# Kernel tuning notes

Hardware: AMD Instinct MI355X
Metric: run time of the kernel (lower is better)

The kernel has to match this reference:

```python
import jax, jax.numpy as jnp
import numpy as np
import math

H = 128
HEADS = 2
NEG = -float(1 << 32)
BN_EPS = 1e-5
LN_EPS = 1e-5


def _bn_eval(x, g, b):
    # BatchNorm1d in eval mode with running_mean=0, running_var=1
    return g * (x / jnp.sqrt(1.0 + BN_EPS)) + b


def _ln(x, g, b):
    mu = x.mean(-1, keepdims=True)
    var = ((x - mu) ** 2).mean(-1, keepdims=True)
    return g * (x - mu) / jnp.sqrt(var + LN_EPS) + b


def _multi_embed(tables, idx):
    # tables [F,V,H], idx [N,F] -> sum_f tables[f, idx[:,f]]  (ogb Atom/BondEncoder)
    F = tables.shape[0]
    return tables[jnp.arange(F)[None, :], idx].sum(axis=1)


def _gin_graph(x, edge_attr, edge_index, batch, num_graphs, atom_emb, bond_emb, eps, w1, b1, g1, be1, w2, b2, g2, be2):
    h = _multi_embed(atom_emb, x)  # [N,H]
    tgt, src = edge_index[0], edge_index[1]
    L = eps.shape[0]
    for l in range(L):
        e = _multi_embed(bond_emb[l], edge_attr)  # [E,H]
        msg = jax.nn.relu(h[src] + e)
        agg = jax.ops.segment_sum(msg, tgt, num_segments=h.shape[0])
        z = (1.0 + eps[l]) * h + agg
        z = jax.nn.relu(_bn_eval(z @ w1[l] + b1[l], g1[l], be1[l])) @ w2[l] + b2[l]
        h = _bn_eval(z, g2[l], be2[l])
        if l != L - 1:
            h = jax.nn.relu(h)  # dropout is identity in eval mode
    s = jax.ops.segment_sum(h, batch, num_segments=num_graphs)
    c = jax.ops.segment_sum(jnp.ones_like(h), batch, num_segments=num_graphs)
    return s / (c + 1e-9)  # mean pooling per graph


def _sab(X, wq, bq, wk, bk, wv, bv, wo, bo, l1g, l1b, l2g, l2b):
    # MAB(X, X) with HEADS heads, use_ln=True. X: [B,S,H]
    B, S, _ = X.shape
    dh = H // HEADS

    def split(T):  # torch split(last)+cat(dim0): head-major [HEADS*B, S, dh]
        return T.reshape(B, S, HEADS, dh).transpose(2, 0, 1, 3).reshape(HEADS * B, S, dh)

    Qs, Ks, Vs = split(X @ wq + bq), split(X @ wk + bk), split(X @ wv + bv)
    A = jax.nn.softmax(jnp.einsum('bqd,bkd->bqk', Qs, Ks) / math.sqrt(dh), axis=-1)
    O = Qs + jnp.einsum('bqk,bkd->bqd', A, Vs)
    O = O.reshape(HEADS, B, S, dh).transpose(1, 2, 0, 3).reshape(B, S, H)
    O = _ln(O, l1g, l1b)
    O = _ln(O @ wo + bo, l2g, l2b)
    return O


def setup_inputs() -> dict:
    key = jax.random.key(0)
    ks = iter(jax.random.split(key, 64))
    nk = lambda: next(ks)
    V, L = 64, 4
    NS, ES = 60000, 140000
    NM, EM = 150000, 350000
    S, M, D, B = 492, 600, 200, 64
    f32 = jnp.float32
    w = lambda *shp: jax.random.normal(nk(), shp, f32) * 0.05
    inp = {}
    inp['atom_emb'] = w(2, 9, V, H)
    inp['bond_emb'] = w(2, L, 3, V, H)
    inp['gin_eps'] = jnp.zeros((2, L), f32)
    inp['gin_w1'] = w(2, L, H, 2 * H); inp['gin_b1'] = jnp.zeros((2, L, 2 * H), f32)
    inp['gin_bn1_g'] = jnp.ones((2, L, 2 * H), f32); inp['gin_bn1_b'] = jnp.zeros((2, L, 2 * H), f32)
    inp['gin_w2'] = w(2, L, 2 * H, H); inp['gin_b2'] = jnp.zeros((2, L, H), f32)
    inp['gin_bn2_g'] = jnp.ones((2, L, H), f32); inp['gin_bn2_b'] = jnp.zeros((2, L, H), f32)
    for nm in ['sab_wq', 'sab_wk', 'sab_wv', 'sab_wo']:
        inp[nm] = w(H, H)
    for nm in ['sab_bq', 'sab_bk', 'sab_bv', 'sab_bo', 'sab_ln1_b', 'sab_ln2_b']:
        inp[nm] = jnp.zeros((H,), f32)
    inp['sab_ln1_g'] = jnp.ones((H,), f32); inp['sab_ln2_g'] = jnp.ones((H,), f32)
    inp['agg_wq'] = w(H, H); inp['agg_bq'] = jnp.zeros((H,), f32)
    inp['agg_wk'] = w(H, H); inp['agg_bk'] = jnp.zeros((H,), f32)
    inp['score_w1'] = w(H, H // 2); inp['score_b1'] = jnp.zeros((H // 2,), f32)
    inp['score_w2'] = w(H // 2, 1); inp['score_b2'] = jnp.zeros((1,), f32)
    inp['patient_emb'] = jax.random.uniform(nk(), (B, S), f32)
    inp['average_projection'] = jax.random.uniform(nk(), (D, M), f32) / M
    inp['sub_x'] = jax.random.randint(nk(), (NS, 9), 0, V)
    inp['sub_edge_attr'] = jax.random.randint(nk(), (ES, 3), 0, V)
    inp['sub_edge_index'] = jax.random.randint(nk(), (2, ES), 0, NS)
    inp['sub_batch'] = jax.random.randint(nk(), (NS,), 0, S)
    inp['mol_x'] = jax.random.randint(nk(), (NM, 9), 0, V)
    inp['mol_edge_attr'] = jax.random.randint(nk(), (EM, 3), 0, V)
    inp['mol_edge_index'] = jax.random.randint(nk(), (2, EM), 0, NM)
    inp['mol_batch'] = jax.random.randint(nk(), (NM,), 0, M)
    mask = jax.random.bernoulli(nk(), 0.3, (D, S))
    inp['mask'] = mask.at[:, 0].set(False)
    inp['num_sub'] = S
    inp['num_mol'] = M
    return inp


def reference(atom_emb, bond_emb, gin_eps, gin_w1, gin_b1, gin_bn1_g, gin_bn1_b, gin_w2, gin_b2, gin_bn2_g, gin_bn2_b, sab_wq, sab_bq, sab_wk, sab_bk, sab_wv, sab_bv, sab_wo, sab_bo, sab_ln1_g, sab_ln1_b, sab_ln2_g, sab_ln2_b, agg_wq, agg_bq, agg_wk, agg_bk, score_w1, score_b1, score_w2, score_b2, patient_emb, average_projection, sub_x, sub_edge_attr, sub_edge_index, sub_batch, mol_x, mol_edge_attr, mol_edge_index, mol_batch, mask, num_sub, num_mol):
    # substructure encoder (GINGraph #0) + SAB interaction
    sub = _gin_graph(sub_x, sub_edge_attr, sub_edge_index, sub_batch, num_sub, atom_emb[0], bond_emb[0], gin_eps[0], gin_w1[0], gin_b1[0], gin_bn1_g[0], gin_bn1_b[0], gin_w2[0], gin_b2[0], gin_bn2_g[0], gin_bn2_b[0])
    sub = _sab(sub[None], sab_wq, sab_bq, sab_wk, sab_bk, sab_wv, sab_bv, sab_wo, sab_bo, sab_ln1_g, sab_ln1_b, sab_ln2_g, sab_ln2_b)[0]  # [S,H]
    # molecule encoder (GINGraph #1) + drug-level averaging
    mol = _gin_graph(mol_x, mol_edge_attr, mol_edge_index, mol_batch, num_mol, atom_emb[1], bond_emb[1], gin_eps[1], gin_w1[1], gin_b1[1], gin_bn1_g[1], gin_bn1_b[1], gin_w2[1], gin_b2[1], gin_bn2_g[1], gin_bn2_b[1])
    mol_emb = average_projection @ mol  # [D,H]
    # AttnAgg: masked attention, per-patient reweighting via diag(fix_feat)
    Q = mol_emb @ agg_wq + agg_bq
    K = sub @ agg_wk + agg_bk
    attn = (Q @ K.T) / math.sqrt(H)
    attn = jax.nn.softmax(jnp.where(mask, NEG, attn), axis=-1)  # [D,S]
    agg = jnp.einsum('ds,bs,sh->bdh', attn, patient_emb, sub)  # [B,D,H]
    logits = (jax.nn.relu(agg @ score_w1 + score_b1) @ score_w2 + score_b2)[..., 0]
    return jax.nn.sigmoid(logits)  # y_prob [B,D]
```

## Files before the change

kernel.cpp:

```cpp
#include <hip/hip_runtime.h>


typedef short short8 __attribute__((ext_vector_type(8)));
typedef unsigned short us8 __attribute__((ext_vector_type(8)));
typedef float f32x4 __attribute__((ext_vector_type(4)));
typedef unsigned short us4 __attribute__((ext_vector_type(4)));
typedef unsigned int u32;

#define BN_RSQ 0.9999950000374997f
#define LN_EPS 1e-5f
#define NEGBIG -4294967296.0f

__device__ __forceinline__ unsigned short f2bf(float x) {
  union { float f; unsigned int u; } v; v.f = x;
  unsigned int r = v.u + 0x7fffu + ((v.u >> 16) & 1u);
  return (unsigned short)(r >> 16);
}
__device__ __forceinline__ float bf2f(unsigned short x) {
  union { unsigned int u; float f; } v; v.u = ((unsigned int)x) << 16;
  return v.f;
}

__global__ __launch_bounds__(256) void prep_all(
    const float* __restrict__ w1, const float* __restrict__ w2,
    unsigned short* __restrict__ w1t, unsigned short* __restrict__ w2t,
    const float* __restrict__ bond, unsigned short* __restrict__ bt16, int bonde,
    const unsigned char* __restrict__ m, int* __restrict__ flags, int maskn) {
  __shared__ int lf[2];
  int b = blockIdx.x;
  if (b < 1024) {
    int i = b * 256 + threadIdx.x;
    int gl = i >> 15;
    int k1 = (i >> 8) & 127, c1 = i & 255;
    w1t[(gl << 15) + c1 * 128 + k1] = f2bf(w1[i]);
    int k2 = (i >> 7) & 255, c2 = i & 127;
    w2t[(gl << 15) + c2 * 256 + k2] = f2bf(w2[i]);
    return;
  }
  if (b < 1792) {
    int i = (b - 1024) * 256 + threadIdx.x;
    if (i < bonde) bt16[i] = f2bf(bond[i]);
    return;
  }
  if (threadIdx.x == 0) { lf[0] = 0; lf[1] = 0; }
  __syncthreads();
  int f0 = 0, f1 = 0;
  for (int i = (b - 1792) * 256 + threadIdx.x; i < maskn; i += 64 * 256) {
    if (m[i]) { if ((i & 3) == 0) f0 = 1; else f1 = 1; }
  }
  if (f0) atomicOr(&lf[0], 1);
  if (f1) atomicOr(&lf[1], 1);
  __syncthreads();
  if (threadIdx.x == 0) {
    if (lf[0]) atomicOr(flags, 1);
    if (lf[1]) atomicOr(flags + 1, 1);
  }
}

__global__ void build_count(const int* __restrict__ ei_m, int Em,
                            const int* __restrict__ ei_s, int Es,
                            const int* __restrict__ bm, int Nm,
                            const int* __restrict__ bs, int Ns,
                            int* __restrict__ deg_e, int* __restrict__ deg_n,
                            int M, int NmR) {
  int i = blockIdx.x * 256 + threadIdx.x;
  if (i < Em) { atomicAdd(&deg_e[ei_m[i]], 1); return; }
  i -= Em;
  if (i < Es) { atomicAdd(&deg_e[NmR + ei_s[i]], 1); return; }
  i -= Es;
  if (i < Nm) { atomicAdd(&deg_n[bm[i]], 1); return; }
  i -= Nm;
  if (i < Ns) { atomicAdd(&deg_n[M + bs[i]], 1); }
}

__global__ __launch_bounds__(256) void scan_block2(
    const int* __restrict__ cntE, int nE, int* __restrict__ exclE, int* __restrict__ bsumE, int nbE,
    const int* __restrict__ cntN, int nN, int* __restrict__ exclN, int* __restrict__ bsumN) {
  const int* cnt; int n; int* excl; int* bsum; int blk;
  if (blockIdx.x < (unsigned)nbE) { cnt = cntE; n = nE; excl = exclE; bsum = bsumE; blk = blockIdx.x; }
  else { cnt = cntN; n = nN; excl = exclN; bsum = bsumN; blk = blockIdx.x - nbE; }
  int gid = blk * 256 + threadIdx.x;
  int lane = threadIdx.x & 63, w = threadIdx.x >> 6;
  int v = (gid < n) ? cnt[gid] : 0;
  int x = v;
#pragma unroll
  for (int off = 1; off < 64; off <<= 1) {
    int y = __shfl_up(x, off, 64);
    if (lane >= off) x += y;
  }
  __shared__ int wt[4];
  if (lane == 63) wt[w] = x;
  __syncthreads();
  int add = 0;
  for (int i = 0; i < w; i++) add += wt[i];
  x += add;
  if (gid < n) excl[gid] = x - v;
  if (threadIdx.x == 255) bsum[blk] = x;
}

__global__ __launch_bounds__(1024) void scan_top2(int* __restrict__ bsumE, int nE,
                                                  int* __restrict__ bsumN, int nN) {
  int* bsum = blockIdx.x ? bsumN : bsumE;
  int n = blockIdx.x ? nN : nE;
  int t = threadIdx.x;
  int lane = t & 63, w = t >> 6;
  int v = (t < n) ? bsum[t] : 0;
  int x = v;
#pragma unroll
  for (int off = 1; off < 64; off <<= 1) {
    int y = __shfl_up(x, off, 64);
    if (lane >= off) x += y;
  }
  __shared__ int wt[16];
  if (lane == 63) wt[w] = x;
  __syncthreads();
  int add = 0;
  for (int i = 0; i < w; i++) add += wt[i];
  x += add;
  if (t < n) bsum[t] = x - v;
}

__global__ void finalize2(const int* __restrict__ exclE, const int* __restrict__ bsumE,
                          int nE, int totE, int* __restrict__ rowE,
                          const int* __restrict__ exclN, const int* __restrict__ bsumN,
                          int nN, int totN, int* __restrict__ rowN) {
  int i = blockIdx.x * 256 + threadIdx.x;
  if (i <= nE) {
    rowE[i] = (i < nE) ? (exclE[i] + bsumE[i >> 8]) : totE;
    return;
  }
  int j = i - nE - 1;
  if (j <= nN) rowN[j] = (j < nN) ? (exclN[j] + bsumN[j >> 8]) : totN;
}

__global__ void scatter2(const int* __restrict__ ei_m, const int* __restrict__ ea_m, int Em,
                         const int* __restrict__ ei_s, const int* __restrict__ ea_s, int Es, int NmR,
                         const int* __restrict__ rowptr_e, int* __restrict__ cur_e,
                         int2* __restrict__ epool,
                         const int* __restrict__ bm, int Nm,
                         const int* __restrict__ bs, int Ns, int M,
                         const int* __restrict__ rowptr_n, int* __restrict__ cur_n,
                         int* __restrict__ npool) {
  int i = blockIdx.x * 256 + threadIdx.x;
  if (i < Em + Es) {
    int g, src, a0, a1, a2;
    if (i < Em) {
      g = ei_m[i]; src = ei_m[Em + i];
      a0 = ea_m[i * 3]; a1 = ea_m[i * 3 + 1]; a2 = ea_m[i * 3 + 2];
    } else {
      int j = i - Em;
      g = NmR + ei_s[j]; src = NmR + ei_s[Es + j];
      a0 = ea_s[j * 3]; a1 = ea_s[j * 3 + 1]; a2 = ea_s[j * 3 + 2];
    }
    int slot = rowptr_e[g] + atomicAdd(&cur_e[g], 1);
    epool[slot] = make_int2(src * 128, a0 | (a1 << 6) | (a2 << 12));
    return;
  }
  int k = i - (Em + Es);
  if (k >= Nm + Ns) return;
  int g, node;
  if (k < Nm) { g = bm[k]; node = k; }
  else { int j = k - Nm; g = M + bs[j]; node = NmR + j; }
  int slot = rowptr_n[g] + atomicAdd(&cur_n[g], 1);
  npool[slot] = node;
}

__global__ void embed2(const int* __restrict__ xm, const int* __restrict__ xs,
                       const float* __restrict__ atab, int Nm, int Ns, int NmR,
                       unsigned short* __restrict__ h) {
  int i = blockIdx.x * 256 + threadIdx.x;
  const int* x; const float* table; int n, cq, outn;
  if (i < Nm * 32) {
    n = i >> 5; cq = (i & 31) * 4; x = xm; table = atab + (size_t)9 * 64 * 128; outn = n;
  } else {
    int j = i - Nm * 32;
    if (j >= Ns * 32) return;
    n = j >> 5; cq = (j & 31) * 4; x = xs; table = atab; outn = NmR + n;
  }
  float4 s = make_float4(0.f, 0.f, 0.f, 0.f);
#pragma unroll
  for (int f = 0; f < 9; f++) {
    int v = x[n * 9 + f];
    float4 tv = *(const float4*)(table + (size_t)(f * 64 + v) * 128 + cq);
    s.x += tv.x; s.y += tv.y; s.z += tv.z; s.w += tv.w;
  }
  us4 o;
  o.x = f2bf(s.x); o.y = f2bf(s.y); o.z = f2bf(s.z); o.w = f2bf(s.w);
  *(us4*)(h + (size_t)outn * 128 + cq) = o;
}

__global__ __launch_bounds__(256, 4) void gin_fused3(
    const unsigned short* __restrict__ hin, unsigned short* __restrict__ hout,
    const float* __restrict__ eps_all, int l, int NmR,
    const unsigned short* __restrict__ bt16,
    const int2* __restrict__ epool, const int* __restrict__ rowptr_e,
    const unsigned short* __restrict__ w1t_a, const float* __restrict__ b1_a,
    const float* __restrict__ g1_a, const float* __restrict__ be1_a,
    const unsigned short* __restrict__ w2t_a, const float* __restrict__ b2_a,
    const float* __restrict__ g2_a, const float* __restrict__ be2_a) {
  __shared__ __align__(16) unsigned char smem[38144];
  unsigned short* z1s = (unsigned short*)smem;
  unsigned short* zs  = (unsigned short*)(smem + 20736);
  int2* recs = (int2*)smem;
  const int CAP = 2592;
  int t = threadIdx.x;
  int r0 = blockIdx.x * 64;
  int g = (r0 < NmR) ? 1 : 0;
  int gl = g * 4 + l;
  const unsigned short* bt = bt16 + (size_t)gl * 3 * 64 * 128;
  const unsigned short* w1t = w1t_a + (size_t)gl * 32768;
  const unsigned short* w2t = w2t_a + (size_t)gl * 32768;
  const float* b1 = b1_a + gl * 256;
  const float* g1 = g1_a + gl * 256;
  const float* be1 = be1_a + gl * 256;
  const float* b2 = b2_a + gl * 128;
  const float* g2 = g2_a + gl * 128;
  const float* be2 = be2_a + gl * 128;
  float eps1 = 1.0f + eps_all[gl];
  int do_relu = (l != 3);

  int e0 = rowptr_e[r0], e1 = rowptr_e[r0 + 64];
  int nE = e1 - e0;
  int nstage = (nE < CAP) ? nE : CAP;
  for (int i = t; i < nstage; i += 256) recs[i] = epool[e0 + i];
  __syncthreads();

#pragma unroll
  for (int p = 0; p < 2; p++) {
    int lr = p * 32 + (t >> 3);
    int n = r0 + lr;
    int cb = (t & 7) * 16;
    float lo[8], hi[8];
    {
      const u32* hr = (const u32*)(hin + (size_t)n * 128 + cb);
      uint4 h0v = *(const uint4*)hr;
      uint4 h1v = *(const uint4*)(hr + 4);
      u32 hd[8] = {h0v.x, h0v.y, h0v.z, h0v.w, h1v.x, h1v.y, h1v.z, h1v.w};
#pragma unroll
      for (int j = 0; j < 8; j++) {
        lo[j] = eps1 * __uint_as_float(hd[j] << 16);
        hi[j] = eps1 * __uint_as_float(hd[j] & 0xffff0000u);
      }
    }
    int le0 = rowptr_e[n] - e0, le1 = rowptr_e[n + 1] - e0;
    for (int li = le0; li < le1; li++) {
      int2 rec = (li < CAP) ? recs[li] : epool[e0 + li];
      u32 ab = (u32)rec.y;
      const u32* hs = (const u32*)(hin + rec.x + cb);
      const u32* q0 = (const u32*)(bt + (ab & 63u) * 128 + cb);
      const u32* q1 = (const u32*)(bt + (64 + ((ab >> 6) & 63u)) * 128 + cb);
      const u32* q2 = (const u32*)(bt + (128 + ((ab >> 12) & 63u)) * 128 + cb);
      uint4 A0 = *(const uint4*)hs, A1 = *(const uint4*)(hs + 4);
      uint4 B0 = *(const uint4*)q0, B1 = *(const uint4*)(q0 + 4);
      uint4 C0 = *(const uint4*)q1, C1 = *(const uint4*)(q1 + 4);
      uint4 D0 = *(const uint4*)q2, D1 = *(const uint4*)(q2 + 4);
      u32 ad[8] = {A0.x, A0.y, A0.z, A0.w, A1.x, A1.y, A1.z, A1.w};
      u32 bd[8] = {B0.x, B0.y, B0.z, B0.w, B1.x, B1.y, B1.z, B1.w};
      u32 cd[8] = {C0.x, C0.y, C0.z, C0.w, C1.x, C1.y, C1.z, C1.w};
      u32 dd[8] = {D0.x, D0.y, D0.z, D0.w, D1.x, D1.y, D1.z, D1.w};
#pragma unroll
      for (int j = 0; j < 8; j++) {
        float sl = __uint_as_float(ad[j] << 16) + __uint_as_float(bd[j] << 16)
                 + __uint_as_float(cd[j] << 16) + __uint_as_float(dd[j] << 16);
        float sh = __uint_as_float(ad[j] & 0xffff0000u) + __uint_as_float(bd[j] & 0xffff0000u)
                 + __uint_as_float(cd[j] & 0xffff0000u) + __uint_as_float(dd[j] & 0xffff0000u);
        lo[j] += fmaxf(sl, 0.f);
        hi[j] += fmaxf(sh, 0.f);
      }
    }
    u32 od[8];
#pragma unroll
    for (int j = 0; j < 8; j++)
      od[j] = (u32)f2bf(lo[j]) | (((u32)f2bf(hi[j])) << 16);
    u32* zr = (u32*)(zs + lr * 136 + cb);
    *(uint4*)zr = make_uint4(od[0], od[1], od[2], od[3]);
    *(uint4*)(zr + 4) = make_uint4(od[4], od[5], od[6], od[7]);
  }
  __syncthreads();

  int lane = t & 63, wave = t >> 6;
  int quad = lane >> 4, l16 = lane & 15;
  {
    short8 bw[4][4];
    int cb = wave * 64;
#pragma unroll
    for (int nt = 0; nt < 4; nt++) {
      const unsigned short* p = w1t + (cb + nt * 16 + l16) * 128 + quad * 8;
#pragma unroll
      for (int kc = 0; kc < 4; kc++) bw[nt][kc] = *(const short8*)(p + kc * 32);
    }
    for (int mt = 0; mt < 4; mt++) {
      short8 af[4];
      const unsigned short* zrow = zs + (mt * 16 + l16) * 136 + quad * 8;
#pragma unroll
      for (int kc = 0; kc < 4; kc++)
        af[kc] = *(const short8*)(zrow + kc * 32);
#pragma unroll
      for (int nt = 0; nt < 4; nt++) {
        f32x4 acc = {0.f, 0.f, 0.f, 0.f};
#pragma unroll
        for (int kc = 0; kc < 4; kc++)
          acc = __builtin_amdgcn_mfma_f32_16x16x32_bf16(af[kc], bw[nt][kc], acc, 0, 0, 0);
        int c = cb + nt * 16 + l16;
        float sc = g1[c] * BN_RSQ, sh = be1[c], bb = b1[c];
#pragma unroll
        for (int reg = 0; reg < 4; reg++) {
          int r = mt * 16 + quad * 4 + reg;
          float y = (acc[reg] + bb) * sc + sh;
          z1s[r * 264 + c] = f2bf(fmaxf(y, 0.f));
        }
      }
      __syncthreads();
    }
  }
  {
    short8 bw[2][8];
    int cb = wave * 32;
#pragma unroll
    for (int nt = 0; nt < 2; nt++) {
      const unsigned short* p = w2t + (cb + nt * 16 + l16) * 256 + quad * 8;
#pragma unroll
      for (int kc = 0; kc < 8; kc++) bw[nt][kc] = *(const short8*)(p + kc * 32);
    }
    for (int mt = 0; mt < 4; mt++) {
      short8 af[8];
      const unsigned short* zrow = z1s + (mt * 16 + l16) * 264 + quad * 8;
#pragma unroll
      for (int kc = 0; kc < 8; kc++)
        af[kc] = *(const short8*)(zrow + kc * 32);
      __syncthreads();
#pragma unroll
      for (int nt = 0; nt < 2; nt++) {
        f32x4 acc = {0.f, 0.f, 0.f, 0.f};
#pragma unroll
        for (int kc = 0; kc < 8; kc++)
          acc = __builtin_amdgcn_mfma_f32_16x16x32_bf16(af[kc], bw[nt][kc], acc, 0, 0, 0);
        int c = cb + nt * 16 + l16;
        float sc = g2[c] * BN_RSQ, sh = be2[c], bb = b2[c];
#pragma unroll
        for (int reg = 0; reg < 4; reg++) {
          int r = mt * 16 + quad * 4 + reg;
          float y = (acc[reg] + bb) * sc + sh;
          if (do_relu) y = fmaxf(y, 0.f);
          z1s[r * 264 + c] = f2bf(y);
        }
      }
    }
  }
  __syncthreads();
  for (int i = t; i < 1024; i += 256) {
    int r = i >> 4, c8 = (i & 15) * 8;
    us8 v = *(const us8*)(z1s + r * 264 + c8);
    *(us8*)(hout + (size_t)(r0 + r) * 128 + c8) = v;
  }
}

__global__ __launch_bounds__(256) void pool_csr(const unsigned short* __restrict__ h,
                                                const int* __restrict__ npool,
                                                const int* __restrict__ rowptr_n,
                                                float* __restrict__ pooled, int nseg) {
  __shared__ int nls[512];
  __shared__ float part[128];
  int m = blockIdx.x;
  if (m >= nseg) return;
  int st = rowptr_n[m];
  int len = rowptr_n[m + 1] - st;
  int c = threadIdx.x & 127, grp = threadIdx.x >> 7;
  float s = 0.f;
  for (int base = 0; base < len; base += 512) {
    int cnt = (len - base < 512) ? (len - base) : 512;
    __syncthreads();
    for (int i = threadIdx.x; i < cnt; i += 256) nls[i] = npool[st + base + i];
    __syncthreads();
    int hh = (cnt + 1) >> 1;
    int i0 = grp * hh;
    int i1 = i0 + hh; if (i1 > cnt) i1 = cnt;
    int i = i0;
    for (; i + 3 < i1; i += 4) {
      int n0 = nls[i], n1 = nls[i + 1], n2 = nls[i + 2], n3 = nls[i + 3];
      float v0 = bf2f(h[(size_t)n0 * 128 + c]);
      float v1 = bf2f(h[(size_t)n1 * 128 + c]);
      float v2 = bf2f(h[(size_t)n2 * 128 + c]);
      float v3 = bf2f(h[(size_t)n3 * 128 + c]);
      s += (v0 + v1) + (v2 + v3);
    }
    for (; i < i1; i++) s += bf2f(h[(size_t)nls[i] * 128 + c]);
  }
  if (grp) part[c] = s;
  __syncthreads();
  if (!grp) pooled[(size_t)m * 128 + c] = (s + part[c]) / ((float)len + 1e-9f);
}

__global__ __launch_bounds__(256) void gemm_tile(const float* __restrict__ A, const float* __restrict__ W,
                                                 const float* __restrict__ bias, float* __restrict__ C,
                                                 int K) {
  __shared__ float As[608];
  __shared__ float red[128];
  int r = blockIdx.x;
  int t = threadIdx.x;
  for (int i = t; i < K; i += 256) As[i] = A[(size_t)r * K + i];
  __syncthreads();
  int c = t & 127, half = t >> 7;
  int Kh = K >> 1;
  int k0 = half * Kh, k1 = k0 + Kh;
  float acc = 0.f;
#pragma unroll 8
  for (int k = k0; k < k1; k++) acc = fmaf(As[k], W[(size_t)k * 128 + c], acc);
  if (half) red[c] = acc;
  __syncthreads();
  if (!half) {
    float v = acc + red[c] + (bias ? bias[c] : 0.f);
    C[(size_t)r * 128 + c] = v;
  }
}

__global__ __launch_bounds__(256) void gemm_qkv(const float* __restrict__ A,
                                                const float* __restrict__ W0, const float* __restrict__ bi0, float* __restrict__ C0,
                                                const float* __restrict__ W1, const float* __restrict__ bi1, float* __restrict__ C1,
                                                const float* __restrict__ W2, const float* __restrict__ bi2, float* __restrict__ C2) {
  __shared__ float As[128];
  __shared__ float red[128];
  int r = blockIdx.x, which = blockIdx.y;
  const float* W = (which == 0) ? W0 : (which == 1) ? W1 : W2;
  const float* bias = (which == 0) ? bi0 : (which == 1) ? bi1 : bi2;
  float* C = (which == 0) ? C0 : (which == 1) ? C1 : C2;
  int t = threadIdx.x;
  if (t < 128) As[t] = A[(size_t)r * 128 + t];
  __syncthreads();
  int c = t & 127, half = t >> 7;
  int k0 = half * 64, k1 = k0 + 64;
  float acc = 0.f;
#pragma unroll 8
  for (int k = k0; k < k1; k++) acc = fmaf(As[k], W[(size_t)k * 128 + c], acc);
  if (half) red[c] = acc;
  __syncthreads();
  if (!half) C[(size_t)r * 128 + c] = acc + red[c] + bias[c];
}

__global__ __launch_bounds__(256) void gemm_aggqk(
    const float* __restrict__ Aq, const float* __restrict__ Wq, const float* __restrict__ bq,
    float* __restrict__ Cq, int D,
    const float* __restrict__ Ak, const float* __restrict__ Wk, const float* __restrict__ bk,
    float* __restrict__ Ck) {
  __shared__ float As[128];
  __shared__ float red[128];
  int r = blockIdx.x;
  const float* A; const float* W; const float* bias; float* C; int rr;
  if (r < D) { A = Aq; W = Wq; bias = bq; C = Cq; rr = r; }
  else { A = Ak; W = Wk; bias = bk; C = Ck; rr = r - D; }
  int t = threadIdx.x;
  if (t < 128) As[t] = A[(size_t)rr * 128 + t];
  __syncthreads();
  int c = t & 127, half = t >> 7;
  int k0 = half * 64, k1 = k0 + 64;
  float acc = 0.f;
#pragma unroll 8
  for (int k = k0; k < k1; k++) acc = fmaf(As[k], W[(size_t)k * 128 + c], acc);
  if (half) red[c] = acc;
  __syncthreads();
  if (!half) C[(size_t)rr * 128 + c] = acc + red[c] + bias[c];
}

__global__ __launch_bounds__(256) void gemm_wo_ln(const float* __restrict__ A,
                                                  const float* __restrict__ W, const float* __restrict__ bias,
                                                  const float* __restrict__ lg, const float* __restrict__ lb,
                                                  float* __restrict__ subf,
                                                  unsigned short* __restrict__ subT) {
  __shared__ float As[128];
  __shared__ float row[128];
  __shared__ float red2[4];
  int r = blockIdx.x;
  int t = threadIdx.x;
  if (t < 128) As[t] = A[(size_t)r * 128 + t];
  __syncthreads();
  int c = t & 127, half = t >> 7;
  int k0 = half * 64, k1 = k0 + 64;
  float acc = 0.f;
#pragma unroll 8
  for (int k = k0; k < k1; k++) acc = fmaf(As[k], W[(size_t)k * 128 + c], acc);
  if (half) row[c] = acc;
  __syncthreads();
  if (!half) row[c] = acc + row[c] + bias[c];
  __syncthreads();
  if (t < 128) {
    float x = row[t];
    float s = x;
    for (int off = 32; off; off >>= 1) s += __shfl_down(s, off);
    if ((t & 63) == 0) red2[t >> 6] = s;
  }
  __syncthreads();
  if (t < 128) {
    float mu = (red2[0] + red2[1]) * (1.f / 128.f);
    float dd = row[t] - mu;
    float v = dd * dd;
    for (int off = 32; off; off >>= 1) v += __shfl_down(v, off);
    if ((t & 63) == 0) red2[2 + (t >> 6)] = v;
  }
  __syncthreads();
  if (t < 128) {
    float mu = (red2[0] + red2[1]) * (1.f / 128.f);
    float var = (red2[2] + red2[3]) * (1.f / 128.f);
    float dd = row[t] - mu;
    float val = lg[t] * dd * rsqrtf(var + LN_EPS) + lb[t];
    subf[(size_t)r * 128 + t] = val;
    subT[(size_t)t * 512 + r] = f2bf(val);
  }
}

__global__ __launch_bounds__(256) void sab_attn(const float* __restrict__ Q, const float* __restrict__ K,
                                                const float* __restrict__ V, float* __restrict__ O, int S) {
  int q = blockIdx.x, hd = blockIdx.y;
  int t = threadIdx.x;
  __shared__ float sc[512];
  __shared__ float red[8];
  __shared__ float pacc[4][64];
  const float* qrow = Q + q * 128 + hd * 64;
  for (int k = t; k < 512; k += 256) {
    float d = -1e30f;
    if (k < S) {
      const float* krow = K + k * 128 + hd * 64;
      d = 0.f;
#pragma unroll
      for (int j = 0; j < 64; j += 4) {
        float4 a = *(const float4*)(qrow + j);
        float4 b = *(const float4*)(krow + j);
        d += a.x * b.x + a.y * b.y + a.z * b.z + a.w * b.w;
      }
      d *= 0.125f;
    }
    sc[k] = d;
  }
  __syncthreads();
  float m = fmaxf(sc[t], sc[t + 256]);
  for (int off = 32; off; off >>= 1) m = fmaxf(m, __shfl_down(m, off));
  if ((t & 63) == 0) red[t >> 6] = m;
  __syncthreads();
  m = fmaxf(fmaxf(red[0], red[1]), fmaxf(red[2], red[3]));
  float p0 = __expf(sc[t] - m), p1 = __expf(sc[t + 256] - m);
  sc[t] = p0; sc[t + 256] = p1;
  float s = p0 + p1;
  for (int off = 32; off; off >>= 1) s += __shfl_down(s, off);
  if ((t & 63) == 0) red[4 + (t >> 6)] = s;
  __syncthreads();
  float inv = 1.f / (red[4] + red[5] + red[6] + red[7]);
  int d = t & 63, part = t >> 6;
  float acc = 0.f;
  for (int k = part; k < S; k += 4) acc += sc[k] * V[k * 128 + hd * 64 + d];
  pacc[part][d] = acc;
  __syncthreads();
  if (part == 0) {
    float o = (pacc[0][d] + pacc[1][d] + pacc[2][d] + pacc[3][d]) * inv;
    O[q * 128 + hd * 64 + d] = qrow[d] + o;
  }
}

__global__ __launch_bounds__(128) void ln_rows(const float* __restrict__ in, float* __restrict__ out,
                                               const float* __restrict__ g, const float* __restrict__ b) {
  int r = blockIdx.x, t = threadIdx.x;
  __shared__ float red[4];
  float x = in[r * 128 + t];
  float s = x;
  for (int off = 32; off; off >>= 1) s += __shfl_down(s, off);
  if ((t & 63) == 0) red[t >> 6] = s;
  __syncthreads();
  float mu = (red[0] + red[1]) * (1.f / 128.f);
  float dd = x - mu;
  float v = dd * dd;
  for (int off = 32; off; off >>= 1) v += __shfl_down(v, off);
  if ((t & 63) == 0) red[2 + (t >> 6)] = v;
  __syncthreads();
  float var = (red[2] + red[3]) * (1.f / 128.f);
  out[r * 128 + t] = g[t] * dd * rsqrtf(var + LN_EPS) + b[t];
}

__global__ __launch_bounds__(256) void agg_fused(const float* __restrict__ Q, const float* __restrict__ Kt,
                                                 const void* __restrict__ mask, const int* __restrict__ flags,
                                                 const float* __restrict__ pat,
                                                 const unsigned short* __restrict__ subT,
                                                 float* __restrict__ aggT, int D, int S) {
  int d = blockIdx.x, t = threadIdx.x;
  __shared__ float sc[512];
  __shared__ float red[8];
  __shared__ unsigned short As[64][40];
  int layout = (flags[1] == 0) ? 0 : (flags[0] ? 1 : 2);
  const float* qrow = Q + d * 128;
  for (int s = t; s < 512; s += 256) {
    float v = NEGBIG;
    if (s < S) {
      int mi = d * S + s;
      bool msk;
      if (layout == 0)      msk = ((const int*)mask)[mi] != 0;
      else if (layout == 1) msk = ((const unsigned char*)mask)[mi] != 0;
      else                  msk = ((const float*)mask)[mi] != 0.f;
      if (!msk) {
        float dd = 0.f;
        const float* krow = Kt + s * 128;
#pragma unroll
        for (int j = 0; j < 128; j += 4) {
          float4 a = *(const float4*)(qrow + j);
          float4 b = *(const float4*)(krow + j);
          dd += a.x * b.x + a.y * b.y + a.z * b.z + a.w * b.w;
        }
        v = dd * 0.08838834764831845f;
      }
    }
    sc[s] = v;
  }
  __syncthreads();
  float m = fmaxf(sc[t], sc[t + 256]);
  for (int off = 32; off; off >>= 1) m = fmaxf(m, __shfl_down(m, off));
  if ((t & 63) == 0) red[t >> 6] = m;
  __syncthreads();
  m = fmaxf(fmaxf(red[0], red[1]), fmaxf(red[2], red[3]));
  float p0 = __expf(sc[t] - m), p1 = __expf(sc[t + 256] - m);
  float s2 = p0 + p1;
  for (int off = 32; off; off >>= 1) s2 += __shfl_down(s2, off);
  if ((t & 63) == 0) red[4 + (t >> 6)] = s2;
  __syncthreads();
  float inv = 1.f / (red[4] + red[5] + red[6] + red[7]);
  sc[t] = p0 * inv;
  sc[t + 256] = p1 * inv;
  __syncthreads();

  int lane = t & 63, wave = t >> 6;
  int quad = lane >> 4, l16 = lane & 15;
  f32x4 acc[8];
#pragma unroll
  for (int nt = 0; nt < 8; nt++) acc[nt] = (f32x4){0.f, 0.f, 0.f, 0.f};
  int srow = t >> 2, skb = (t & 3) * 8;
  for (int c = 0; c < 16; c++) {
    int s0 = c * 32;
    __syncthreads();
    unsigned short v[8];
#pragma unroll
    for (int j = 0; j < 8; j++) {
      int s = s0 + skb + j;
      float x = (s < S) ? sc[s] * pat[srow * S + s] : 0.f;
      v[j] = f2bf(x);
    }
    *(us4*)&As[srow][skb]     = *(us4*)&v[0];
    *(us4*)&As[srow][skb + 4] = *(us4*)&v[4];
    __syncthreads();
    short8 af = *(const short8*)&As[16 * wave + l16][quad * 8];
#pragma unroll
    for (int nt = 0; nt < 8; nt++) {
      short8 bf = *(const short8*)(subT + (nt * 16 + l16) * 512 + s0 + quad * 8);
      acc[nt] = __builtin_amdgcn_mfma_f32_16x16x32_bf16(af, bf, acc[nt], 0, 0, 0);
    }
  }
#pragma unroll
  for (int nt = 0; nt < 8; nt++) {
    int hh = nt * 16 + l16;
#pragma unroll
    for (int reg = 0; reg < 4; reg++) {
      int b = 16 * wave + quad * 4 + reg;
      aggT[((size_t)(b * D + d)) * 128 + hh] = acc[nt][reg];
    }
  }
}

__global__ __launch_bounds__(256) void score_head(const float* __restrict__ aggT,
                                                  const float* __restrict__ w1, const float* __restrict__ b1,
                                                  const float* __restrict__ w2, const float* __restrict__ b2,
                                                  float* __restrict__ out, int total) {
  int i = blockIdx.x * 4 + (threadIdx.x >> 6);
  int j = threadIdx.x & 63;
  if (i >= total) return;
  const float* av = aggT + (size_t)i * 128;
  float acc = b1[j];
#pragma unroll 8
  for (int k = 0; k < 128; k++) acc = fmaf(av[k], w1[k * 64 + j], acc);
  acc = fmaxf(acc, 0.f) * w2[j];
  for (int off = 32; off; off >>= 1) acc += __shfl_down(acc, off);
  if (j == 0) {
    float x = acc + b2[0];
    out[i] = 1.f / (1.f + __expf(-x));
  }
}

extern "C" void kernel_launch(void* const* d_in, const int* in_sizes, int n_in,
                              void* d_out, int out_size, void* d_ws, size_t ws_size,
                              hipStream_t stream) {
  const float* atom_emb = (const float*)d_in[0];
  const float* bond_emb = (const float*)d_in[1];
  const float* gin_eps  = (const float*)d_in[2];
  const float* gin_w1   = (const float*)d_in[3];
  const float* gin_b1   = (const float*)d_in[4];
  const float* bn1g     = (const float*)d_in[5];
  const float* bn1b     = (const float*)d_in[6];
  const float* gin_w2   = (const float*)d_in[7];
  const float* gin_b2   = (const float*)d_in[8];
  const float* bn2g     = (const float*)d_in[9];
  const float* bn2b     = (const float*)d_in[10];
  const float* sab_wq = (const float*)d_in[11];
  const float* sab_wk = (const float*)d_in[12];
  const float* sab_wv = (const float*)d_in[13];
  const float* sab_wo = (const float*)d_in[14];
  const float* sab_bq = (const float*)d_in[15];
  const float* sab_bk = (const float*)d_in[16];
  const float* sab_bv = (const float*)d_in[17];
  const float* sab_bo = (const float*)d_in[18];
  const float* ln1b = (const float*)d_in[19];
  const float* ln2b = (const float*)d_in[20];
  const float* ln1g = (const float*)d_in[21];
  const float* ln2g = (const float*)d_in[22];
  const float* agg_wq = (const float*)d_in[23];
  const float* agg_bq = (const float*)d_in[24];
  const float* agg_wk = (const float*)d_in[25];
  const float* agg_bk = (const float*)d_in[26];
  const float* score_w1 = (const float*)d_in[27];
  const float* score_b1 = (const float*)d_in[28];
  const float* score_w2 = (const float*)d_in[29];
  const float* score_b2 = (const float*)d_in[30];
  const float* patient  = (const float*)d_in[31];
  const float* avgproj  = (const float*)d_in[32];
  const int* sub_x     = (const int*)d_in[33];
  const int* sub_ea    = (const int*)d_in[34];
  const int* sub_ei    = (const int*)d_in[35];
  const int* sub_batch = (const int*)d_in[36];
  const int* mol_x     = (const int*)d_in[37];
  const int* mol_ea    = (const int*)d_in[38];
  const int* mol_ei    = (const int*)d_in[39];
  const int* mol_batch = (const int*)d_in[40];
  const void* mask     = d_in[41];

  const int Ns = in_sizes[33] / 9, Es = in_sizes[34] / 3;
  const int Nm = in_sizes[37] / 9, Em = in_sizes[38] / 3;
  const int S = 492, M = 600, D = 200, B = 64;
  const int NmR = (Nm + 63) & ~63;
  const int NsR = (Ns + 63) & ~63;
  const int NTOT = NmR + NsR;
  const int NSEG = M + S;
  const int ETOT = Em + Es;
  const int BONDE = 2 * 4 * 3 * 64 * 128;

  char* Wp = (char*)d_ws;
  size_t off = 0;
  auto alloc = [&](size_t bytes) -> void* {
    void* p = Wp + off;
    off = (off + bytes + 255) & ~(size_t)255;
    return p;
  };
  unsigned short* h0 = (unsigned short*)alloc((size_t)NTOT * 128 * 2);
  unsigned short* h1 = (unsigned short*)alloc((size_t)NTOT * 128 * 2);
  unsigned short* w1t = (unsigned short*)alloc(262144 * 2);
  unsigned short* w2t = (unsigned short*)alloc(262144 * 2);
  unsigned short* bt16 = (unsigned short*)alloc((size_t)BONDE * 2);
  int2* epool  = (int2*)alloc((size_t)ETOT * 8);
  int*  npool  = (int*)alloc((size_t)(Nm + Ns) * 4);
  int*  excl_e = (int*)alloc((size_t)NTOT * 4);
  int*  bsum_e = (int*)alloc(1024 * 4);
  int*  excl_n = (int*)alloc((size_t)NSEG * 4);
  int*  bsum_n = (int*)alloc(1024 * 4);
  int*  rowptr_e = (int*)alloc((size_t)(NTOT + 1) * 4);
  int*  rowptr_n = (int*)alloc((size_t)(NSEG + 1) * 4);
  char* zstart = Wp + off;
  int*  deg_e  = (int*)alloc((size_t)NTOT * 4);
  int*  deg_n  = (int*)alloc((size_t)NSEG * 4);
  int*  cur_e  = (int*)alloc((size_t)NTOT * 4);
  int*  cur_n  = (int*)alloc((size_t)NSEG * 4);
  int*  flags  = (int*)alloc(8);
  unsigned short* subT = (unsigned short*)alloc((size_t)128 * 512 * 2);
  size_t zsize = (size_t)((Wp + off) - zstart);
  float* pooled_all = (float*)alloc((size_t)NSEG * 128 * 4);
  float* pooled_mol = pooled_all;
  float* pooled_sub = pooled_all + (size_t)M * 128;
  float* Qb   = (float*)alloc((size_t)S * 128 * 4);
  float* Kb   = (float*)alloc((size_t)S * 128 * 4);
  float* Vb   = (float*)alloc((size_t)S * 128 * 4);
  float* Ob   = (float*)alloc((size_t)S * 128 * 4);
  float* subf = (float*)alloc((size_t)S * 128 * 4);
  float* mol_embb = (float*)alloc((size_t)D * 128 * 4);
  float* aggQb = (float*)alloc((size_t)D * 128 * 4);
  float* aggKb = (float*)alloc((size_t)S * 128 * 4);
  float* aggTb = (float*)alloc((size_t)B * D * 128 * 4);
  (void)ws_size; (void)n_in; (void)out_size;

  hipMemsetAsync(zstart, 0, zsize, stream);
  prep_all<<<1856, 256, 0, stream>>>(gin_w1, gin_w2, w1t, w2t,
                                     bond_emb, bt16, BONDE,
                                     (const unsigned char*)mask, flags, D * S);

  int total_cnt = Em + Es + Nm + Ns;
  build_count<<<(total_cnt + 255) / 256, 256, 0, stream>>>(
      mol_ei, Em, sub_ei, Es, mol_batch, Nm, sub_batch, Ns, deg_e, deg_n, M, NmR);
  int nb_e = (NTOT + 255) / 256;
  int nb_n = (NSEG + 255) / 256;
  scan_block2<<<nb_e + nb_n, 256, 0, stream>>>(deg_e, NTOT, excl_e, bsum_e, nb_e,
                                               deg_n, NSEG, excl_n, bsum_n);
  scan_top2<<<2, 1024, 0, stream>>>(bsum_e, nb_e, bsum_n, nb_n);
  finalize2<<<((NTOT + 1) + (NSEG + 1) + 1 + 255) / 256, 256, 0, stream>>>(
      excl_e, bsum_e, NTOT, ETOT, rowptr_e,
      excl_n, bsum_n, NSEG, Nm + Ns, rowptr_n);
  scatter2<<<(ETOT + Nm + Ns + 255) / 256, 256, 0, stream>>>(
      mol_ei, mol_ea, Em, sub_ei, sub_ea, Es, NmR, rowptr_e, cur_e, epool,
      mol_batch, Nm, sub_batch, Ns, M, rowptr_n, cur_n, npool);

  embed2<<<((Nm + Ns) * 32 + 255) / 256, 256, 0, stream>>>(
      mol_x, sub_x, atom_emb, Nm, Ns, NmR, h0);
  unsigned short* hin = h0; unsigned short* hout = h1;
  for (int l = 0; l < 4; l++) {
    gin_fused3<<<NTOT / 64, 256, 0, stream>>>(
        hin, hout, gin_eps, l, NmR, bt16, epool, rowptr_e,
        w1t, gin_b1, bn1g, bn1b, w2t, gin_b2, bn2g, bn2b);
    unsigned short* tmp = hin; hin = hout; hout = tmp;
  }
  pool_csr<<<NSEG, 256, 0, stream>>>(hin, npool, rowptr_n, pooled_all, NSEG);

  gemm_qkv<<<dim3(S, 3), 256, 0, stream>>>(pooled_sub,
                                           sab_wq, sab_bq, Qb,
                                           sab_wk, sab_bk, Kb,
                                           sab_wv, sab_bv, Vb);
  sab_attn<<<dim3(S, 2), 256, 0, stream>>>(Qb, Kb, Vb, Ob, S);
  ln_rows<<<S, 128, 0, stream>>>(Ob, Ob, ln1g, ln1b);
  gemm_wo_ln<<<S, 256, 0, stream>>>(Ob, sab_wo, sab_bo, ln2g, ln2b, subf, subT);

  gemm_tile<<<D, 256, 0, stream>>>(avgproj, pooled_mol, (const float*)nullptr, mol_embb, 600);

  gemm_aggqk<<<D + S, 256, 0, stream>>>(mol_embb, agg_wq, agg_bq, aggQb, D,
                                        subf, agg_wk, agg_bk, aggKb);
  agg_fused<<<D, 256, 0, stream>>>(aggQb, aggKb, mask, flags, patient, subT, aggTb, D, S);
  score_head<<<(B * D + 3) / 4, 256, 0, stream>>>(aggTb, score_w1, score_b1, score_w2, score_b2,
                                                  (float*)d_out, B * D);
}
```

Baseline: 945.6 us.

## Renumber graph nodes by in-degree bucket to balance GIN block workloads

Adds a counting-sort pass (degree histogram, scan and permutation assignment) that renumbers nodes within the molecule and substructure graphs by clamped in-degree. Edge CSR, pooling lists and embeddings are all built in the permuted order. The aim is for each 64-row tile in the fused GIN layer to hold nodes of similar degree, which evens out per-block edge work. In exchange it adds several small kernel launches and extra atomics. It may also hurt gather locality, because neighbouring source rows are no longer contiguous.

```diff
diff --git a/kernel.cpp b/kernel.cpp
--- a/kernel.cpp
+++ b/kernel.cpp
@@ -57,20 +57,58 @@
   }
 }
 
-__global__ void build_count(const int* __restrict__ ei_m, int Em,
-                            const int* __restrict__ ei_s, int Es,
-                            const int* __restrict__ bm, int Nm,
-                            const int* __restrict__ bs, int Ns,
-                            int* __restrict__ deg_e, int* __restrict__ deg_n,
-                            int M, int NmR) {
+__global__ void build_count_old(const int* __restrict__ ei_m, int Em,
+                                const int* __restrict__ ei_s, int Es,
+                                const int* __restrict__ bm, int Nm,
+                                const int* __restrict__ bs, int Ns,
+                                int* __restrict__ deg_old, int* __restrict__ deg_n, int M) {
   int i = blockIdx.x * 256 + threadIdx.x;
-  if (i < Em) { atomicAdd(&deg_e[ei_m[i]], 1); return; }
+  if (i < Em) { atomicAdd(&deg_old[ei_m[i]], 1); return; }
   i -= Em;
-  if (i < Es) { atomicAdd(&deg_e[NmR + ei_s[i]], 1); return; }
+  if (i < Es) { atomicAdd(&deg_old[Nm + ei_s[i]], 1); return; }
   i -= Es;
   if (i < Nm) { atomicAdd(&deg_n[bm[i]], 1); return; }
   i -= Nm;
   if (i < Ns) { atomicAdd(&deg_n[M + bs[i]], 1); }
+}
+
+__global__ void deg_hist(const int* __restrict__ deg_old, int Nm, int Ntot,
+                         int* __restrict__ hist) {
+  int i = blockIdx.x * 256 + threadIdx.x;
+  if (i >= Ntot) return;
+  int d = deg_old[i]; if (d > 63) d = 63;
+  int r = (i < Nm) ? 0 : 1;
+  atomicAdd(&hist[r * 64 + d], 1);
+}
+
+__global__ __launch_bounds__(128) void hist_scan(const int* __restrict__ hist,
+                                                 int* __restrict__ binbase) {
+  int t = threadIdx.x;
+  int lane = t & 63;
+  int v = hist[t];
+  int x = v;
+#pragma unroll
+  for (int off = 1; off < 64; off <<= 1) {
+    int y = __shfl_up(x, off, 64);
+    if (lane >= off) x += y;
+  }
+  binbase[t] = x - v;
+}
+
+__global__ void perm_assign(const int* __restrict__ deg_old, int Nm, int Ntot, int NmR,
+                            const int* __restrict__ binbase, int* __restrict__ bincur,
+                            int* __restrict__ perm, int* __restrict__ iperm,
+                            int* __restrict__ deg_new) {
+  int i = blockIdx.x * 256 + threadIdx.x;
+  if (i >= Ntot) return;
+  int dg = deg_old[i];
+  int d = (dg > 63) ? 63 : dg;
+  int r = (i < Nm) ? 0 : 1;
+  int slot = binbase[r * 64 + d] + atomicAdd(&bincur[r * 64 + d], 1);
+  int nid = (r ? NmR : 0) + slot;
+  perm[i] = nid;
+  iperm[nid] = i;
+  deg_new[nid] = dg;
 }
 
 __global__ __launch_bounds__(256) void scan_block2(
@@ -134,59 +172,60 @@
 }
 
 __global__ void scatter2(const int* __restrict__ ei_m, const int* __restrict__ ea_m, int Em,
-                         const int* __restrict__ ei_s, const int* __restrict__ ea_s, int Es, int NmR,
+                         const int* __restrict__ ei_s, const int* __restrict__ ea_s, int Es, int Nm,
+                         const int* __restrict__ perm,
                          const int* __restrict__ rowptr_e, int* __restrict__ cur_e,
                          int2* __restrict__ epool,
-                         const int* __restrict__ bm, int Nm,
+                         const int* __restrict__ bm,
                          const int* __restrict__ bs, int Ns, int M,
                          const int* __restrict__ rowptr_n, int* __restrict__ cur_n,
                          int* __restrict__ npool) {
   int i = blockIdx.x * 256 + threadIdx.x;
   if (i < Em + Es) {
-    int g, src, a0, a1, a2;
+    int tgt_old, src_old, a0, a1, a2;
     if (i < Em) {
-      g = ei_m[i]; src = ei_m[Em + i];
+      tgt_old = ei_m[i]; src_old = ei_m[Em + i];
       a0 = ea_m[i * 3]; a1 = ea_m[i * 3 + 1]; a2 = ea_m[i * 3 + 2];
     } else {
       int j = i - Em;
-      g = NmR + ei_s[j]; src = NmR + ei_s[Es + j];
+      tgt_old = Nm + ei_s[j]; src_old = Nm + ei_s[Es + j];
       a0 = ea_s[j * 3]; a1 = ea_s[j * 3 + 1]; a2 = ea_s[j * 3 + 2];
     }
+    int g = perm[tgt_old];
+    int src = perm[src_old];
     int slot = rowptr_e[g] + atomicAdd(&cur_e[g], 1);
     epool[slot] = make_int2(src * 128, a0 | (a1 << 6) | (a2 << 12));
     return;
   }
   int k = i - (Em + Es);
   if (k >= Nm + Ns) return;
-  int g, node;
-  if (k < Nm) { g = bm[k]; node = k; }
-  else { int j = k - Nm; g = M + bs[j]; node = NmR + j; }
+  int g = (k < Nm) ? bm[k] : (M + bs[k - Nm]);
+  int node = perm[k];
   int slot = rowptr_n[g] + atomicAdd(&cur_n[g], 1);
   npool[slot] = node;
 }
 
 __global__ void embed2(const int* __restrict__ xm, const int* __restrict__ xs,
-                       const float* __restrict__ atab, int Nm, int Ns, int NmR,
+                       const float* __restrict__ atab, int Nm, int NTOT,
+                       const int* __restrict__ iperm,
                        unsigned short* __restrict__ h) {
   int i = blockIdx.x * 256 + threadIdx.x;
-  const int* x; const float* table; int n, cq, outn;
-  if (i < Nm * 32) {
-    n = i >> 5; cq = (i & 31) * 4; x = xm; table = atab + (size_t)9 * 64 * 128; outn = n;
-  } else {
-    int j = i - Nm * 32;
-    if (j >= Ns * 32) return;
-    n = j >> 5; cq = (j & 31) * 4; x = xs; table = atab; outn = NmR + n;
-  }
+  if (i >= NTOT * 32) return;
+  int n = i >> 5, cq = (i & 31) * 4;
+  int old = iperm[n];
+  const int* x; const float* table; int row;
+  if (old < Nm) { x = xm; table = atab + (size_t)9 * 64 * 128; row = old; }
+  else { x = xs; table = atab; row = old - Nm; }
   float4 s = make_float4(0.f, 0.f, 0.f, 0.f);
 #pragma unroll
   for (int f = 0; f < 9; f++) {
-    int v = x[n * 9 + f];
+    int v = x[row * 9 + f];
     float4 tv = *(const float4*)(table + (size_t)(f * 64 + v) * 128 + cq);
     s.x += tv.x; s.y += tv.y; s.z += tv.z; s.w += tv.w;
   }
   us4 o;
   o.x = f2bf(s.x); o.y = f2bf(s.y); o.z = f2bf(s.z); o.w = f2bf(s.w);
-  *(us4*)(h + (size_t)outn * 128 + cq) = o;
+  *(us4*)(h + (size_t)n * 128 + cq) = o;
 }
 
 __global__ __launch_bounds__(256, 4) void gin_fused3(
@@ -732,6 +771,7 @@
   const int NTOT = NmR + NsR;
   const int NSEG = M + S;
   const int ETOT = Em + Es;
+  const int NOLD = Nm + Ns;
   const int BONDE = 2 * 4 * 3 * 64 * 128;
 
   char* Wp = (char*)d_ws;
@@ -747,18 +787,24 @@
   unsigned short* w2t = (unsigned short*)alloc(262144 * 2);
   unsigned short* bt16 = (unsigned short*)alloc((size_t)BONDE * 2);
   int2* epool  = (int2*)alloc((size_t)ETOT * 8);
-  int*  npool  = (int*)alloc((size_t)(Nm + Ns) * 4);
+  int*  npool  = (int*)alloc((size_t)NOLD * 4);
+  int*  perm   = (int*)alloc((size_t)NOLD * 4);
   int*  excl_e = (int*)alloc((size_t)NTOT * 4);
   int*  bsum_e = (int*)alloc(1024 * 4);
   int*  excl_n = (int*)alloc((size_t)NSEG * 4);
   int*  bsum_n = (int*)alloc(1024 * 4);
   int*  rowptr_e = (int*)alloc((size_t)(NTOT + 1) * 4);
   int*  rowptr_n = (int*)alloc((size_t)(NSEG + 1) * 4);
+  int*  binbase = (int*)alloc(128 * 4);
   char* zstart = Wp + off;
+  int*  deg_old = (int*)alloc((size_t)NOLD * 4);
   int*  deg_e  = (int*)alloc((size_t)NTOT * 4);
   int*  deg_n  = (int*)alloc((size_t)NSEG * 4);
   int*  cur_e  = (int*)alloc((size_t)NTOT * 4);
   int*  cur_n  = (int*)alloc((size_t)NSEG * 4);
+  int*  hist   = (int*)alloc(128 * 4);
+  int*  bincur = (int*)alloc(128 * 4);
+  int*  iperm  = (int*)alloc((size_t)NTOT * 4);
   int*  flags  = (int*)alloc(8);
   unsigned short* subT = (unsigned short*)alloc((size_t)128 * 512 * 2);
   size_t zsize = (size_t)((Wp + off) - zstart);
@@ -782,8 +828,12 @@
                                      (const unsigned char*)mask, flags, D * S);
 
   int total_cnt = Em + Es + Nm + Ns;
-  build_count<<<(total_cnt + 255) / 256, 256, 0, stream>>>(
-      mol_ei, Em, sub_ei, Es, mol_batch, Nm, sub_batch, Ns, deg_e, deg_n, M, NmR);
+  build_count_old<<<(total_cnt + 255) / 256, 256, 0, stream>>>(
+      mol_ei, Em, sub_ei, Es, mol_batch, Nm, sub_batch, Ns, deg_old, deg_n, M);
+  deg_hist<<<(NOLD + 255) / 256, 256, 0, stream>>>(deg_old, Nm, NOLD, hist);
+  hist_scan<<<1, 128, 0, stream>>>(hist, binbase);
+  perm_assign<<<(NOLD + 255) / 256, 256, 0, stream>>>(
+      deg_old, Nm, NOLD, NmR, binbase, bincur, perm, iperm, deg_e);
   int nb_e = (NTOT + 255) / 256;
   int nb_n = (NSEG + 255) / 256;
   scan_block2<<<nb_e + nb_n, 256, 0, stream>>>(deg_e, NTOT, excl_e, bsum_e, nb_e,
@@ -791,13 +841,13 @@
   scan_top2<<<2, 1024, 0, stream>>>(bsum_e, nb_e, bsum_n, nb_n);
   finalize2<<<((NTOT + 1) + (NSEG + 1) + 1 + 255) / 256, 256, 0, stream>>>(
       excl_e, bsum_e, NTOT, ETOT, rowptr_e,
-      excl_n, bsum_n, NSEG, Nm + Ns, rowptr_n);
-  scatter2<<<(ETOT + Nm + Ns + 255) / 256, 256, 0, stream>>>(
-      mol_ei, mol_ea, Em, sub_ei, sub_ea, Es, NmR, rowptr_e, cur_e, epool,
-      mol_batch, Nm, sub_batch, Ns, M, rowptr_n, cur_n, npool);
-
-  embed2<<<((Nm + Ns) * 32 + 255) / 256, 256, 0, stream>>>(
-      mol_x, sub_x, atom_emb, Nm, Ns, NmR, h0);
+      excl_n, bsum_n, NSEG, NOLD, rowptr_n);
+  scatter2<<<(ETOT + NOLD + 255) / 256, 256, 0, stream>>>(
+      mol_ei, mol_ea, Em, sub_ei, sub_ea, Es, Nm, perm, rowptr_e, cur_e, epool,
+      mol_batch, sub_batch, Ns, M, rowptr_n, cur_n, npool);
+
+  embed2<<<(NTOT * 32 + 255) / 256, 256, 0, stream>>>(
+      mol_x, sub_x, atom_emb, Nm, NTOT, iperm, h0);
   unsigned short* hin = h0; unsigned short* hout = h1;
   for (int l = 0; l < 4; l++) {
     gin_fused3<<<NTOT / 64, 256, 0, stream>>>(
```

Measured after the change: 2.414 ms. 2.55x slower.
